# Kernel optimization log

Measured on AMD Instinct MI355X. Metric: run time of the kernel, lower is better.

## Reference

```python
import jax, jax.numpy as jnp
import numpy as np

B, S, D = 4, 8192, 1024
EPS = 5e-05  # var_add scalar from the torch module


def setup_inputs() -> dict:
    key = jax.random.key(0)
    k_x, k_w, k_b = jax.random.split(key, 3)
    x = jax.random.normal(k_x, (B, S, D), dtype=jnp.float32)
    weight = jax.random.uniform(k_w, (D,), dtype=jnp.float32)
    bias = jax.random.normal(k_b, (D,), dtype=jnp.float32)
    return {"x": x, "weight": weight, "bias": bias}


def _loop(inp, x):
    # Faithful to QLayerNorm.loop: (input / x + x) * 0.5 (quant/dequant stubs are identity)
    return (inp / x + x) * 0.5


def reference(x, weight, bias):
    # LayerNorm with explicit mean/var reduction and a 4-step Newton-style sqrt,
    # exactly mirroring the torch forward (including its argument ordering in loop()).
    mean = jnp.mean(x, axis=-1, keepdims=True)           # [B,S,1]
    mean_sub = x - mean                                  # [B,S,D]
    var = jnp.mean(mean_sub * mean_sub, axis=-1, keepdims=True)  # [B,S,1]
    a = var + EPS
    l1 = _loop(a, a)
    l2 = _loop(l1, a)
    l3 = _loop(l2, a)
    std = _loop(l3, a)
    return (mean_sub / std) * weight + bias
```

## Files before the change

kernel.cpp:

```cpp
#include <hip/hip_runtime.h>


constexpr int D_DIM = 1024;
constexpr float EPS = 5e-5f;

__global__ __launch_bounds__(256) void qln_kernel(
    const float* __restrict__ x,
    const float* __restrict__ w,
    const float* __restrict__ b,
    float* __restrict__ out,
    int nrows)
{
    const int gtid = blockIdx.x * blockDim.x + threadIdx.x;
    const int row  = gtid >> 6;
    const int lane = gtid & 63;
    if (row >= nrows) return;

    const float4* __restrict__ xr = (const float4*)(x + (size_t)row * D_DIM);

    float4 v[4];
    float sum = 0.f, sq = 0.f;
#pragma unroll
    for (int c = 0; c < 4; ++c) {
        v[c] = xr[lane + 64 * c];
        sum += (v[c].x + v[c].y) + (v[c].z + v[c].w);
        sq = fmaf(v[c].x, v[c].x, sq);
        sq = fmaf(v[c].y, v[c].y, sq);
        sq = fmaf(v[c].z, v[c].z, sq);
        sq = fmaf(v[c].w, v[c].w, sq);
    }

#pragma unroll
    for (int m = 32; m >= 1; m >>= 1) {
        sum += __shfl_xor(sum, m, 64);
        sq  += __shfl_xor(sq,  m, 64);
    }

    const float invD = 1.0f / (float)D_DIM;
    const float mean = sum * invD;
    const float var  = fmaf(-mean, mean, sq * invD);
    const float a    = var + EPS;

    float l = (a / a + a) * 0.5f;
    l = (l / a + a) * 0.5f;
    l = (l / a + a) * 0.5f;
    const float std_ = (l / a + a) * 0.5f;
    const float inv_std = 1.0f / std_;

    const float4* __restrict__ w4 = (const float4*)w;
    const float4* __restrict__ b4 = (const float4*)b;
    float4* __restrict__ orow = (float4*)(out + (size_t)row * D_DIM);

#pragma unroll
    for (int c = 0; c < 4; ++c) {
        const float4 wv = w4[lane + 64 * c];
        const float4 bv = b4[lane + 64 * c];
        float4 ov;
        ov.x = fmaf((v[c].x - mean) * inv_std, wv.x, bv.x);
        ov.y = fmaf((v[c].y - mean) * inv_std, wv.y, bv.y);
        ov.z = fmaf((v[c].z - mean) * inv_std, wv.z, bv.z);
        ov.w = fmaf((v[c].w - mean) * inv_std, wv.w, bv.w);
        orow[lane + 64 * c] = ov;
    }
}

extern "C" void kernel_launch(void* const* d_in, const int* in_sizes, int n_in,
                              void* d_out, int out_size, void* d_ws, size_t ws_size,
                              hipStream_t stream) {
    const float* x = (const float*)d_in[0];
    const float* w = (const float*)d_in[1];
    const float* b = (const float*)d_in[2];
    float* out = (float*)d_out;

    const int nrows = in_sizes[0] / D_DIM;
    const int threads = 256;
    const int blocks = (nrows * 64) / threads;
    qln_kernel<<<blocks, threads, 0, stream>>>(x, w, b, out, nrows);
}
```

Before: 232.0 us.

## Process two rows per wave with nontemporal loads/stores and hoisted weight/bias

```diff
diff --git a/kernel.cpp b/kernel.cpp
--- a/kernel.cpp
+++ b/kernel.cpp
@@ -3,6 +3,8 @@
 
 constexpr int D_DIM = 1024;
 constexpr float EPS = 5e-5f;
+
+typedef float vfloat4 __attribute__((ext_vector_type(4)));
 
 __global__ __launch_bounds__(256) void qln_kernel(
     const float* __restrict__ x,
@@ -12,55 +14,101 @@
     int nrows)
 {
     const int gtid = blockIdx.x * blockDim.x + threadIdx.x;
-    const int row  = gtid >> 6;
+    const int wid  = gtid >> 6;
     const int lane = gtid & 63;
-    if (row >= nrows) return;
+    const int r0 = wid * 2;
+    const int r1 = r0 + 1;
+    if (r0 >= nrows) return;
+    const bool has2 = (r1 < nrows);
 
-    const float4* __restrict__ xr = (const float4*)(x + (size_t)row * D_DIM);
+    const vfloat4* __restrict__ w4 = (const vfloat4*)w;
+    const vfloat4* __restrict__ b4 = (const vfloat4*)b;
+    const vfloat4* __restrict__ xr0 = (const vfloat4*)(x + (size_t)r0 * D_DIM);
+    const vfloat4* __restrict__ xr1 = (const vfloat4*)(x + (size_t)r1 * D_DIM);
 
-    float4 v[4];
-    float sum = 0.f, sq = 0.f;
+    vfloat4 wv[4], bv[4];
 #pragma unroll
     for (int c = 0; c < 4; ++c) {
-        v[c] = xr[lane + 64 * c];
-        sum += (v[c].x + v[c].y) + (v[c].z + v[c].w);
-        sq = fmaf(v[c].x, v[c].x, sq);
-        sq = fmaf(v[c].y, v[c].y, sq);
-        sq = fmaf(v[c].z, v[c].z, sq);
-        sq = fmaf(v[c].w, v[c].w, sq);
+        wv[c] = w4[lane + 64 * c];
+        bv[c] = b4[lane + 64 * c];
+    }
+
+    vfloat4 v0[4], v1[4];
+#pragma unroll
+    for (int c = 0; c < 4; ++c)
+        v0[c] = __builtin_nontemporal_load(&xr0[lane + 64 * c]);
+    if (has2) {
+#pragma unroll
+        for (int c = 0; c < 4; ++c)
+            v1[c] = __builtin_nontemporal_load(&xr1[lane + 64 * c]);
+    } else {
+#pragma unroll
+        for (int c = 0; c < 4; ++c) v1[c] = (vfloat4)(0.f);
+    }
+
+    float sum0 = 0.f, sq0 = 0.f, sum1 = 0.f, sq1 = 0.f;
+#pragma unroll
+    for (int c = 0; c < 4; ++c) {
+        sum0 += (v0[c].x + v0[c].y) + (v0[c].z + v0[c].w);
+        sq0 = fmaf(v0[c].x, v0[c].x, sq0);
+        sq0 = fmaf(v0[c].y, v0[c].y, sq0);
+        sq0 = fmaf(v0[c].z, v0[c].z, sq0);
+        sq0 = fmaf(v0[c].w, v0[c].w, sq0);
+        sum1 += (v1[c].x + v1[c].y) + (v1[c].z + v1[c].w);
+        sq1 = fmaf(v1[c].x, v1[c].x, sq1);
+        sq1 = fmaf(v1[c].y, v1[c].y, sq1);
+        sq1 = fmaf(v1[c].z, v1[c].z, sq1);
+        sq1 = fmaf(v1[c].w, v1[c].w, sq1);
     }
 
 #pragma unroll
     for (int m = 32; m >= 1; m >>= 1) {
-        sum += __shfl_xor(sum, m, 64);
-        sq  += __shfl_xor(sq,  m, 64);
+        sum0 += __shfl_xor(sum0, m, 64);
+        sq0  += __shfl_xor(sq0,  m, 64);
+        sum1 += __shfl_xor(sum1, m, 64);
+        sq1  += __shfl_xor(sq1,  m, 64);
     }
 
     const float invD = 1.0f / (float)D_DIM;
-    const float mean = sum * invD;
-    const float var  = fmaf(-mean, mean, sq * invD);
-    const float a    = var + EPS;
+    const float mean0 = sum0 * invD;
+    const float mean1 = sum1 * invD;
+    const float var0 = fmaf(-mean0, mean0, sq0 * invD);
+    const float var1 = fmaf(-mean1, mean1, sq1 * invD);
+    const float a0 = var0 + EPS;
+    const float a1 = var1 + EPS;
 
-    float l = (a / a + a) * 0.5f;
-    l = (l / a + a) * 0.5f;
-    l = (l / a + a) * 0.5f;
-    const float std_ = (l / a + a) * 0.5f;
-    const float inv_std = 1.0f / std_;
+    float l0 = (a0 / a0 + a0) * 0.5f;
+    float l1 = (a1 / a1 + a1) * 0.5f;
+    l0 = (l0 / a0 + a0) * 0.5f;
+    l1 = (l1 / a1 + a1) * 0.5f;
+    l0 = (l0 / a0 + a0) * 0.5f;
+    l1 = (l1 / a1 + a1) * 0.5f;
+    const float std0 = (l0 / a0 + a0) * 0.5f;
+    const float std1 = (l1 / a1 + a1) * 0.5f;
+    const float is0 = 1.0f / std0;
+    const float is1 = 1.0f / std1;
 
-    const float4* __restrict__ w4 = (const float4*)w;
-    const float4* __restrict__ b4 = (const float4*)b;
-    float4* __restrict__ orow = (float4*)(out + (size_t)row * D_DIM);
-
+    vfloat4* __restrict__ o0 = (vfloat4*)(out + (size_t)r0 * D_DIM);
 #pragma unroll
     for (int c = 0; c < 4; ++c) {
-        const float4 wv = w4[lane + 64 * c];
-        const float4 bv = b4[lane + 64 * c];
-        float4 ov;
-        ov.x = fmaf((v[c].x - mean) * inv_std, wv.x, bv.x);
-        ov.y = fmaf((v[c].y - mean) * inv_std, wv.y, bv.y);
-        ov.z = fmaf((v[c].z - mean) * inv_std, wv.z, bv.z);
-        ov.w = fmaf((v[c].w - mean) * inv_std, wv.w, bv.w);
-        orow[lane + 64 * c] = ov;
+        vfloat4 ov;
+        ov.x = fmaf((v0[c].x - mean0) * is0, wv[c].x, bv[c].x);
+        ov.y = fmaf((v0[c].y - mean0) * is0, wv[c].y, bv[c].y);
+        ov.z = fmaf((v0[c].z - mean0) * is0, wv[c].z, bv[c].z);
+        ov.w = fmaf((v0[c].w - mean0) * is0, wv[c].w, bv[c].w);
+        __builtin_nontemporal_store(ov, &o0[lane + 64 * c]);
+    }
+    if (has2) {
+        vfloat4* __restrict__ o1 = (vfloat4*)(out + (size_t)r1 * D_DIM);
+#pragma unroll
+        for (int c = 0; c < 4; ++c) {
+            vfloat4 ov;
+            ov.x = fmaf((v1[c].x - mean1) * is1, wv[c].x, bv[c].x);
+            ov.y = fmaf((v1[c].y - mean1) * is1, wv[c].y, bv[c].y);
+            ov.z = fmaf((v1[c].z - mean1) * is1, wv[c].z, bv[c].z);
+            ov.w = fmaf((v1[c].w - mean1) * is1, wv[c].w, bv[c].w);
+            __builtin_nontemporal_store(ov, &o1[lane + 64 * c]);
+        }
     }
 }
 
@@ -73,7 +121,8 @@
     float* out = (float*)d_out;
 
     const int nrows = in_sizes[0] / D_DIM;
+    const int nwaves = (nrows + 1) / 2;
     const int threads = 256;
-    const int blocks = (nrows * 64) / threads;
+    const int blocks = (nwaves * 64 + threads - 1) / threads;
     qln_kernel<<<blocks, threads, 0, stream>>>(x, w, b, out, nrows);
 }
```

Result: faster. 224.3 us (-3.3%).
